# Optimization experiments

Measured on AMD Instinct MI355X. Metric: run time of the kernel, lower is better.

Reference implementation:

```python
import jax, jax.numpy as jnp
import numpy as np

B, N, M, H, NH = 8, 1024, 512, 1024, 4
DH = H // NH          # 256 main attention head size
CDH = (H // 4) // 4   # 64  cross attention qk head size
EPS = 1e-12


def _ln(x, g, b):
    mu = jnp.mean(x, axis=-1, keepdims=True)
    var = jnp.mean((x - mu) ** 2, axis=-1, keepdims=True)
    return (x - mu) / jnp.sqrt(var + EPS) * g + b


def _heads(x, nh):
    b, n, d = x.shape
    return x.reshape(b, n, nh, d // nh).transpose(0, 2, 1, 3)  # [b,nh,n,dh]


def setup_inputs() -> dict:
    key = jax.random.key(0)
    ks = iter(jax.random.split(key, 64))
    nk = lambda: next(ks)
    w = lambda *s: jax.random.normal(nk(), s, jnp.float32) * 0.02
    inp = {}
    inp["hidden_states"] = jax.random.normal(nk(), (B, N, H), jnp.float32)
    inp["attention_mask"] = jnp.ones((B, N), jnp.float32)
    inp["structure_mask"] = (jax.random.uniform(nk(), (B, 3, N, N)) < 0.2).astype(jnp.float32)
    inp["Sentence_em"] = w(1, B, N, H)
    inp["entity_id_em"] = w(1, B, N, H)
    inp["cross_struct_mask"] = (jax.random.uniform(nk(), (B, 1, N, M)) < 0.3).astype(jnp.float32)
    inp["encoder_hidden_states"] = jax.random.normal(nk(), (1, B, M, H), jnp.float32)
    inp["encoder_attention_mask"] = jnp.ones((B, M), jnp.float32)
    # ---- Struct_SelfAttention params ----
    inp["Wq"] = w(H, 3 * DH); inp["bq"] = jnp.zeros(3 * DH)
    inp["Wk"] = w(H, 3 * DH); inp["bk"] = jnp.zeros(3 * DH)
    inp["Wv"] = w(H, H);      inp["bv"] = jnp.zeros(H)
    inp["Wq1"] = w(H, DH);    inp["bq1"] = jnp.zeros(DH)
    inp["Wk1"] = w(H, DH);    inp["bk1"] = jnp.zeros(DH)
    inp["ln_g"] = jnp.ones(H); inp["ln_b"] = jnp.zeros(H)
    inp["gnn_W"] = w(H, H); inp["gnn_b"] = jnp.zeros(H)
    inp["gnn_ln_g"] = jnp.ones(H); inp["gnn_ln_b"] = jnp.zeros(H)
    # ---- Cross_Attention params ----
    inp["cWq"] = w(H, H // 4); inp["cbq"] = jnp.zeros(H // 4)
    inp["cWk"] = w(H, H // 4); inp["cbk"] = jnp.zeros(H // 4)
    inp["cWv"] = w(H, H);      inp["cbv"] = jnp.zeros(H)
    inp["cWo"] = w(H, H);      inp["cbo"] = jnp.zeros(H)
    inp["cWg"] = w(2 * H, H);  inp["cbg"] = jnp.full((H,), -1.0, jnp.float32)  # Gate bias init -1
    inp["c_ln_g"] = jnp.ones(H); inp["c_ln_b"] = jnp.zeros(H)
    # ---- Output block params ----
    inp["oW1"] = w(H, H); inp["ob1"] = jnp.zeros(H)
    inp["o_ln1_g"] = jnp.ones(H); inp["o_ln1_b"] = jnp.zeros(H)
    inp["oW2"] = w(H, 2 * H); inp["ob2"] = jnp.zeros(2 * H)
    inp["oW3"] = w(2 * H, H); inp["ob3"] = jnp.zeros(H)
    inp["o_ln3_g"] = jnp.ones(H); inp["o_ln3_b"] = jnp.zeros(H)
    inp["layer_idx"] = 0
    return inp


def reference(hidden_states, attention_mask, structure_mask, Sentence_em, entity_id_em,
              cross_struct_mask, encoder_hidden_states, encoder_attention_mask,
              Wq, bq, Wk, bk, Wv, bv, Wq1, bq1, Wk1, bk1, ln_g, ln_b,
              gnn_W, gnn_b, gnn_ln_g, gnn_ln_b,
              cWq, cbq, cWk, cbk, cWv, cbv, cWo, cbo, cWg, cbg, c_ln_g, c_ln_b,
              oW1, ob1, o_ln1_g, o_ln1_b, oW2, ob2, oW3, ob3, o_ln3_g, o_ln3_b,
              layer_idx):
    hs = hidden_states
    q = _heads(hs @ Wq + bq, 3)          # [B,3,N,DH]
    k = _heads(hs @ Wk + bk, 3)
    v = _heads(hs @ Wv + bv, 4)          # [B,4,N,DH]
    s1 = jnp.einsum('bhnd,bhmd->bhnm', q, k)          # unscaled scores, 3 heads
    am0 = (1.0 - attention_mask)[:, None, None, :] * -10000.0
    s3 = s1 + am0
    # valid off-diagonal pairs mask (broadcasts over the 3 heads)
    pair = attention_mask[:, None, :, None] * attention_mask[:, None, None, :]
    idxw = ((pair * (1.0 - jnp.eye(N, dtype=jnp.float32))) > 0.5).astype(jnp.float32)  # [B,1,N,N]
    # sigmoid focal loss (gamma=2, alpha=0.25, mean over selected elements)
    p = jax.nn.sigmoid(s3)
    t = structure_mask
    fl = 0.25 * t * (1.0 - p) ** 2 * (-jax.nn.log_sigmoid(s3)) \
       + 0.75 * (1.0 - t) * p ** 2 * (-jax.nn.log_sigmoid(-s3))
    loss = jnp.sum(fl * idxw) / (3.0 * jnp.sum(idxw))
    # structural attention path (3 heads)
    s1 = s1 / np.float32(np.sqrt(DH)) + (1.0 - structure_mask) * -10000.0
    probs1 = jax.nn.softmax(s1, axis=-1)
    # positional/structural single-head path
    h1 = _ln(hs + Sentence_em[layer_idx] + entity_id_em[layer_idx], ln_g, ln_b)
    q1 = _heads(h1 @ Wq1 + bq1, 1)
    k1 = _heads(h1 @ Wk1 + bk1, 1)
    s2 = jnp.einsum('bhnd,bhmd->bhnm', q1, k1) / np.float32(np.sqrt(DH)) + am0
    probs2 = jax.nn.softmax(s2, axis=-1)
    probs = jnp.concatenate([probs2, probs1], axis=1)  # [B,4,N,N]
    ctx = jnp.einsum('bhnm,bhmd->bhnd', probs, v).transpose(0, 2, 1, 3).reshape(B, N, H)
    gnn_out = _ln(ctx @ gnn_W + gnn_b, gnn_ln_g, gnn_ln_b)
    # ---- Cross attention ----
    enc = encoder_hidden_states[layer_idx]            # [B,M,H]
    cq = _heads(gnn_out @ cWq + cbq, 4)               # [B,4,N,CDH]
    ck = _heads(enc @ cWk + cbk, 4)                   # [B,4,M,CDH]
    cv = _heads(enc @ cWv + cbv, 4)                   # [B,4,M,DH]
    cs = jnp.einsum('bhnd,bhmd->bhnm', cq, ck) / np.float32(np.sqrt(CDH))
    cs = cs + (1.0 - cross_struct_mask) * -10000.0
    cp = jax.nn.softmax(cs, axis=-1)
    cctx = jnp.einsum('bhnm,bhmd->bhnd', cp, cv).transpose(0, 2, 1, 3).reshape(B, N, H)
    cctx = cctx @ cWo + cbo
    gate = jax.nn.sigmoid(jnp.concatenate([gnn_out, cctx], axis=-1) @ cWg + cbg)
    cross_out = _ln(gate * cctx + (1.0 - gate) * gnn_out, c_ln_g, c_ln_b)
    # ---- Output block (gated FFN) ----
    h = _ln(cross_out @ oW1 + ob1 + hidden_states, o_ln1_g, o_ln1_b)
    h3 = jax.nn.gelu(h @ oW2 + ob2, approximate=False) @ oW3 + ob3
    out = _ln(h3 + h, o_ln3_g, o_ln3_b)
    return out, loss
```

## Files before the change

### kernel.cpp

```cpp
#include <hip/hip_runtime.h>
#include <math.h>

#define DEV __device__ __forceinline__

typedef short short8 __attribute__((ext_vector_type(8)));
typedef float float4v __attribute__((ext_vector_type(4)));

DEV unsigned short f2bf(float f) {
    union { float f; unsigned u; } v; v.f = f;
    unsigned r = v.u + 0x7FFFu + ((v.u >> 16) & 1u);
    return (unsigned short)(r >> 16);
}

DEV void async16(const unsigned short* g, unsigned short* l) {
    __builtin_amdgcn_global_load_lds(
        (const __attribute__((address_space(1))) unsigned int*)g,
        (__attribute__((address_space(3))) unsigned int*)l, 16, 0, 0);
}

DEV float block_reduce(float v, int mode) {
    #pragma unroll
    for (int off = 32; off; off >>= 1) {
        float o = __shfl_xor(v, off);
        v = mode ? fmaxf(v, o) : (v + o);
    }
    __shared__ float sbuf[4];
    __syncthreads();
    if ((threadIdx.x & 63) == 0) sbuf[threadIdx.x >> 6] = v;
    __syncthreads();
    float r = sbuf[0];
    #pragma unroll
    for (int w = 1; w < 4; w++) r = mode ? fmaxf(r, sbuf[w]) : (r + sbuf[w]);
    return r;
}

template <bool BIAS, bool ACCUM, bool GELU>
__global__ __launch_bounds__(256) void gemm_bf16_kernel(
    const unsigned short* __restrict__ A, int lda,
    const unsigned short* __restrict__ Bt, int ldb,
    const float* __restrict__ bias, const float* __restrict__ bias2,
    const float* __restrict__ bias3, int ns1, int ns2,
    float* __restrict__ Cf, unsigned short* __restrict__ Cb,
    int N, int Nb, int K)
{
    __shared__ unsigned short As[128 * 32];
    __shared__ unsigned short Bs[128 * 32];
    const int tid = threadIdx.x;
    const int w = tid >> 6, lane = tid & 63;
    const int l15 = lane & 15, quad = lane >> 4;
    const int m0 = blockIdx.y * 128, n0 = blockIdx.x * 128;
    const int wm = (w >> 1) * 64, wn = (w & 1) * 64;
    const int lr = lane >> 2, lc = (lane & 3) * 8;

    float4v acc[4][4];
    #pragma unroll
    for (int i = 0; i < 4; i++)
        #pragma unroll
        for (int j = 0; j < 4; j++) acc[i][j] = (float4v){0.f, 0.f, 0.f, 0.f};

    const unsigned short* Ab = A  + (size_t)(m0 + w * 16 + lr) * lda + lc;
    const unsigned short* Bb = Bt + (size_t)(n0 + w * 16 + lr) * ldb + lc;
    unsigned short* AsW = As + (w * 16) * 32;
    unsigned short* BsW = Bs + (w * 16) * 32;

    for (int k0 = 0; k0 < K; k0 += 32) {
        __syncthreads();
        async16(Ab + k0, AsW);
        async16(Ab + (size_t)64 * lda + k0, AsW + 64 * 32);
        async16(Bb + k0, BsW);
        async16(Bb + (size_t)64 * ldb + k0, BsW + 64 * 32);
        __syncthreads();
        short8 Af[4], Bf[4];
        #pragma unroll
        for (int mt = 0; mt < 4; mt++)
            Af[mt] = *(const short8*)(As + (wm + mt * 16 + l15) * 32 + quad * 8);
        #pragma unroll
        for (int nt = 0; nt < 4; nt++)
            Bf[nt] = *(const short8*)(Bs + (wn + nt * 16 + l15) * 32 + quad * 8);
        #pragma unroll
        for (int mt = 0; mt < 4; mt++)
            #pragma unroll
            for (int nt = 0; nt < 4; nt++)
                acc[mt][nt] = __builtin_amdgcn_mfma_f32_16x16x32_bf16(
                    Af[mt], Bf[nt], acc[mt][nt], 0, 0, 0);
    }

    #pragma unroll
    for (int nt = 0; nt < 4; nt++) {
        const int n = n0 + wn + nt * 16 + l15;
        float bv = 0.f;
        if (BIAS) bv = (n < ns1) ? bias[n] : (n < ns2) ? bias2[n - ns1]
                                                       : bias3[n - ns2];
        #pragma unroll
        for (int mt = 0; mt < 4; mt++) {
            #pragma unroll
            for (int r = 0; r < 4; r++) {
                const int m = m0 + wm + mt * 16 + quad * 4 + r;
                const size_t off = (size_t)m * N + n;
                float v = acc[mt][nt][r] + bv;
                if (ACCUM) v += Cf[off];
                if (GELU) v = 0.5f * v * (1.f + erff(v * 0.70710678118654752f));
                if (Cf) Cf[off] = v;
                if (Cb) Cb[(size_t)m * Nb + n] = f2bf(v);
            }
        }
    }
}

__global__ __launch_bounds__(256) void wtrans_kernel(
    const float* __restrict__ W, unsigned short* __restrict__ Wt, int K, int N)
{
    __shared__ float t[32][33];
    const int n0 = blockIdx.x * 32, k0 = blockIdx.y * 32;
    const int c = threadIdx.x & 31, r8 = threadIdx.x >> 5;
    #pragma unroll
    for (int i = 0; i < 4; i++) {
        const int r = r8 + i * 8;
        t[r][c] = W[(size_t)(k0 + r) * N + n0 + c];
    }
    __syncthreads();
    #pragma unroll
    for (int i = 0; i < 4; i++) {
        const int r = r8 + i * 8;
        Wt[(size_t)(n0 + r) * K + k0 + c] = f2bf(t[c][r]);
    }
}

__global__ __launch_bounds__(256) void trans_kernel(
    const unsigned short* __restrict__ v, unsigned short* __restrict__ Vt,
    int R, int C, int vpitch, int voff)
{
    __shared__ unsigned short t[32][33];
    const int b = blockIdx.z, r0 = blockIdx.x * 32, c0 = blockIdx.y * 32;
    const int c = threadIdx.x & 31, r8 = threadIdx.x >> 5;
    #pragma unroll
    for (int i = 0; i < 4; i++) {
        const int r = r8 + i * 8;
        t[r][c] = v[((size_t)b * R + r0 + r) * vpitch + voff + c0 + c];
    }
    __syncthreads();
    #pragma unroll
    for (int i = 0; i < 4; i++) {
        const int r = r8 + i * 8;
        Vt[((size_t)b * C + c0 + r) * R + r0 + c] = t[c][r];
    }
}

__global__ __launch_bounds__(256) void castbf_kernel(
    const float* __restrict__ x, unsigned short* __restrict__ y)
{
    const size_t i = ((size_t)blockIdx.x * 256 + threadIdx.x) * 4;
    float4 v = *(const float4*)(x + i);
    ushort4 o;
    o.x = f2bf(v.x); o.y = f2bf(v.y); o.z = f2bf(v.z); o.w = f2bf(v.w);
    *(ushort4*)(y + i) = o;
}

__global__ __launch_bounds__(256) void packmask_kernel(
    const float* __restrict__ x, unsigned int* __restrict__ bits)
{
    const size_t idx = (size_t)blockIdx.x * 256 + threadIdx.x;
    const unsigned long long m = __ballot(x[idx] > 0.5f);
    const int lane = threadIdx.x & 63;
    if (lane == 0)  bits[idx >> 5] = (unsigned)m;
    if (lane == 32) bits[idx >> 5] = (unsigned)(m >> 32);
}

DEV void ln_finish(float4 xv, const float* __restrict__ g,
                   const float* __restrict__ bb, float* __restrict__ outf,
                   unsigned short* __restrict__ outb, size_t base_f, size_t base_b)
{
    float s  = xv.x + xv.y + xv.z + xv.w;
    float s2 = xv.x * xv.x + xv.y * xv.y + xv.z * xv.z + xv.w * xv.w;
    #pragma unroll
    for (int off = 32; off; off >>= 1) {
        s += __shfl_xor(s, off);
        s2 += __shfl_xor(s2, off);
    }
    __shared__ float sa[4], sb[4];
    if ((threadIdx.x & 63) == 0) {
        sa[threadIdx.x >> 6] = s; sb[threadIdx.x >> 6] = s2;
    }
    __syncthreads();
    s  = sa[0] + sa[1] + sa[2] + sa[3];
    s2 = sb[0] + sb[1] + sb[2] + sb[3];
    const float mu  = s * (1.f / 1024.f);
    const float var = fmaxf(s2 * (1.f / 1024.f) - mu * mu, 0.f);
    const float inv = rsqrtf(var + 1e-12f);
    const int tid = threadIdx.x;
    float4 gv = ((const float4*)g)[tid];
    float4 bv = ((const float4*)bb)[tid];
    float4 o;
    o.x = (xv.x - mu) * inv * gv.x + bv.x;
    o.y = (xv.y - mu) * inv * gv.y + bv.y;
    o.z = (xv.z - mu) * inv * gv.z + bv.z;
    o.w = (xv.w - mu) * inv * gv.w + bv.w;
    if (outf) ((float4*)(outf + base_f))[tid] = o;
    if (outb) {
        ushort4 ob;
        ob.x = f2bf(o.x); ob.y = f2bf(o.y); ob.z = f2bf(o.z); ob.w = f2bf(o.w);
        ((ushort4*)(outb + base_b))[tid] = ob;
    }
}

__global__ __launch_bounds__(256) void ln_kernel(
    const float* __restrict__ x, const float* __restrict__ r1,
    const float* __restrict__ r2, const float* __restrict__ g,
    const float* __restrict__ bb, float* __restrict__ outf,
    unsigned short* __restrict__ outb, int obp)
{
    const size_t base = (size_t)blockIdx.x * 1024;
    const size_t base_b = (size_t)blockIdx.x * obp;
    const int tid = threadIdx.x;
    float4 xv = ((const float4*)(x + base))[tid];
    if (r1) {
        float4 a = ((const float4*)(r1 + base))[tid];
        xv.x += a.x; xv.y += a.y; xv.z += a.z; xv.w += a.w;
    }
    if (r2) {
        float4 a = ((const float4*)(r2 + base))[tid];
        xv.x += a.x; xv.y += a.y; xv.z += a.z; xv.w += a.w;
    }
    ln_finish(xv, g, bb, outf, outb, base, base_b);
}

__global__ __launch_bounds__(256) void gate_ln_kernel(
    const float* __restrict__ gpre, const float* __restrict__ co,
    const float* __restrict__ gn, const float* __restrict__ g,
    const float* __restrict__ bb, float* __restrict__ outf,
    unsigned short* __restrict__ outb)
{
    const size_t base = (size_t)blockIdx.x * 1024;
    const int tid = threadIdx.x;
    float4 gp = ((const float4*)(gpre + base))[tid];
    float4 cv = ((const float4*)(co + base))[tid];
    float4 gv = ((const float4*)(gn + base))[tid];
    float4 xv; float s;
    s = 1.f / (1.f + __expf(-gp.x)); xv.x = s * cv.x + (1.f - s) * gv.x;
    s = 1.f / (1.f + __expf(-gp.y)); xv.y = s * cv.y + (1.f - s) * gv.y;
    s = 1.f / (1.f + __expf(-gp.z)); xv.z = s * cv.z + (1.f - s) * gv.z;
    s = 1.f / (1.f + __expf(-gp.w)); xv.w = s * cv.w + (1.f - s) * gv.w;
    ln_finish(xv, g, bb, outf, outb, base, base);
}

__global__ __launch_bounds__(256) void attn_mfma_kernel(
    const unsigned short* __restrict__ qkv,
    const unsigned short* __restrict__ q1k1,
    const unsigned short* __restrict__ Vt,
    const float* __restrict__ am,
    const unsigned int* __restrict__ smb,
    unsigned short* __restrict__ ctx,
    float* __restrict__ nump, float* __restrict__ denp)
{
    const int bid0 = blockIdx.x + 16 * blockIdx.y + 64 * blockIdx.z;
    const int xcd = bid0 & 7, s = bid0 >> 3;
    const int grp = xcd + 8 * (s >> 4);
    const int nb = s & 15;
    const int h = grp & 3, b = grp >> 2;
    const int tid = threadIdx.x;
    const int w = tid >> 6, lane = tid & 63;
    const int l15 = lane & 15, quad = lane >> 4;
    const int n0 = nb * 64;

    __shared__ unsigned short Ks[32 * 264];
    __shared__ unsigned short Vs[256 * 40];
    __shared__ unsigned short Ps[4][16 * 40];

    const unsigned short* qsrc; const unsigned short* ksrc; int pitch;
    if (h == 0) { qsrc = q1k1;                ksrc = q1k1 + 256;                pitch = 512; }
    else        { qsrc = qkv + (h - 1) * 256; ksrc = qkv + 768 + (h - 1) * 256; pitch = 2560; }

    short8 Qf[8];
    {
        const unsigned short* qrow =
            qsrc + (size_t)(b * 1024 + n0 + w * 16 + l15) * pitch;
        #pragma unroll
        for (int kk = 0; kk < 8; kk++)
            Qf[kk] = *(const short8*)(qrow + kk * 32 + quad * 8);
    }

    float4v O[16];
    #pragma unroll
    for (int i = 0; i < 16; i++) O[i] = (float4v){0.f, 0.f, 0.f, 0.f};
    float lsum[4] = {0.f, 0.f, 0.f, 0.f};
    float flsum = 0.f, dencnt = 0.f;
    const int nrow_base = n0 + w * 16 + quad * 4;
    const float* amrow = am + b * 1024;
    float amn[4];
    #pragma unroll
    for (int r = 0; r < 4; r++) amn[r] = amrow[nrow_base + r];
    const unsigned int* smw = (h > 0)
        ? smb + ((size_t)(b * 3 + (h - 1)) << 15) : nullptr;
    const int vrow0 = b * 1024 + h * 256;

    for (int m0 = 0; m0 < 1024; m0 += 32) {
        __syncthreads();
        for (int c = tid; c < 1024; c += 256) {
            const int row = c >> 5, kc = (c & 31) * 8;
            *(uint4*)(Ks + row * 264 + kc) =
                *(const uint4*)(ksrc + (size_t)(b * 1024 + m0 + row) * pitch + kc);
        }
        for (int c = tid; c < 1024; c += 256) {
            const int d = c >> 2, mc = (c & 3) * 8;
            *(uint4*)(Vs + d * 40 + mc) =
                *(const uint4*)(Vt + (size_t)(vrow0 + d) * 1024 + m0 + mc);
        }
        __syncthreads();

        float4v S[2];
        #pragma unroll
        for (int st = 0; st < 2; st++) {
            float4v a = (float4v){0.f, 0.f, 0.f, 0.f};
            #pragma unroll
            for (int kk = 0; kk < 8; kk++) {
                short8 Kf = *(const short8*)(Ks + (st * 16 + l15) * 264 + kk * 32 + quad * 8);
                a = __builtin_amdgcn_mfma_f32_16x16x32_bf16(Qf[kk], Kf, a, 0, 0, 0);
            }
            S[st] = a;
        }

        unsigned int wb[4];
        if (h > 0) {
            #pragma unroll
            for (int r = 0; r < 4; r++)
                wb[r] = smw[(size_t)(nrow_base + r) * 32 + (m0 >> 5)];
        }

        float e[2][4];
        #pragma unroll
        for (int st = 0; st < 2; st++) {
            const int mcol = m0 + st * 16 + l15;
            const float amm = amrow[mcol];
            const float am0 = (1.f - amm) * (-10000.f);
            #pragma unroll
            for (int r = 0; r < 4; r++) {
                const float sraw = S[st][r];
                float scv;
                if (h > 0) {
                    const float t = (float)((wb[r] >> (st * 16 + l15)) & 1u);
                    const int nrow = nrow_base + r;
                    const float s3 = sraw + am0;
                    const float idxw =
                        ((amn[r] * amm * ((mcol == nrow) ? 0.f : 1.f)) > 0.5f) ? 1.f : 0.f;
                    const float E = __expf(-fabsf(s3));
                    const float L = __logf(1.f + E);
                    const float R = 1.f / (1.f + E);
                    const float p = (s3 >= 0.f) ? R : E * R;
                    const float sp = fmaxf(s3, 0.f) + L;
                    const float omp = 1.f - p;
                    flsum += idxw * (0.25f * t * omp * omp * (sp - s3)
                                   + 0.75f * (1.f - t) * p * p * sp);
                    dencnt += idxw;
                    scv = sraw * 0.0625f + (1.f - t) * (-10000.f);
                } else {
                    scv = sraw * 0.0625f + am0;
                }
                const float ev = __expf(fminf(scv, 30.f));
                e[st][r] = ev;
                lsum[r] += ev;
            }
        }

        #pragma unroll
        for (int st = 0; st < 2; st++)
            #pragma unroll
            for (int r = 0; r < 4; r++)
                Ps[w][(quad * 4 + r) * 40 + st * 16 + l15] = f2bf(e[st][r]);
        const short8 Pf = *(const short8*)(&Ps[w][l15 * 40 + quad * 8]);
        #pragma unroll
        for (int dt = 0; dt < 16; dt++) {
            short8 Vf = *(const short8*)(Vs + (dt * 16 + l15) * 40 + quad * 8);
            O[dt] = __builtin_amdgcn_mfma_f32_16x16x32_bf16(Pf, Vf, O[dt], 0, 0, 0);
        }
    }

    float rinv[4];
    #pragma unroll
    for (int r = 0; r < 4; r++) {
        float s2 = lsum[r];
        #pragma unroll
        for (int off = 8; off; off >>= 1) s2 += __shfl_xor(s2, off);
        rinv[r] = 1.f / s2;
    }
    #pragma unroll
    for (int dt = 0; dt < 16; dt++)
        #pragma unroll
        for (int r = 0; r < 4; r++)
            ctx[(size_t)(b * 1024 + nrow_base + r) * 1024 + h * 256 + dt * 16 + l15]
                = f2bf(O[dt][r] * rinv[r]);

    if (h > 0) {
        const float fb = block_reduce(flsum, 0);
        if (tid == 0) nump[(b * 3 + (h - 1)) * 16 + nb] = fb;
        if (h == 1) {
            const float db = block_reduce(dencnt, 0);
            if (tid == 0) denp[b * 16 + nb] = db;
        }
    }
}

__global__ __launch_bounds__(256) void cross_mfma_kernel(
    const unsigned short* __restrict__ cq,
    const unsigned short* __restrict__ ckv,
    const unsigned short* __restrict__ cvt,
    const unsigned int* __restrict__ csmb,
    unsigned short* __restrict__ cctx)
{
    const int bid0 = blockIdx.x + 16 * blockIdx.y + 64 * blockIdx.z;
    const int xcd = bid0 & 7, s = bid0 >> 3;
    const int grp = xcd + 8 * (s >> 4);
    const int nb = s & 15;
    const int h = grp & 3, b = grp >> 2;
    const int tid = threadIdx.x;
    const int w = tid >> 6, lane = tid & 63;
    const int l15 = lane & 15, quad = lane >> 4;
    const int n0 = nb * 64;

    __shared__ unsigned short Ks[32 * 72];
    __shared__ unsigned short Vs[256 * 40];
    __shared__ unsigned short Ps[4][16 * 40];

    short8 Qf[2];
    {
        const unsigned short* qrow =
            cq + (size_t)(b * 1024 + n0 + w * 16 + l15) * 256 + h * 64;
        #pragma unroll
        for (int kk = 0; kk < 2; kk++)
            Qf[kk] = *(const short8*)(qrow + kk * 32 + quad * 8);
    }

    float4v O[16];
    #pragma unroll
    for (int i = 0; i < 16; i++) O[i] = (float4v){0.f, 0.f, 0.f, 0.f};
    float lsum[4] = {0.f, 0.f, 0.f, 0.f};
    const int nrow_base = n0 + w * 16 + quad * 4;
    const unsigned int* csw = csmb + (size_t)(b * 1024) * 16;
    const int vrow0 = b * 1024 + h * 256;

    for (int m0 = 0; m0 < 512; m0 += 32) {
        __syncthreads();
        {
            const int row = tid >> 3, kc = (tid & 7) * 8;
            *(uint4*)(Ks + row * 72 + kc) =
                *(const uint4*)(ckv + (size_t)(b * 512 + m0 + row) * 1280 + h * 64 + kc);
        }
        for (int c = tid; c < 1024; c += 256) {
            const int d = c >> 2, mc = (c & 3) * 8;
            *(uint4*)(Vs + d * 40 + mc) =
                *(const uint4*)(cvt + (size_t)(vrow0 + d) * 512 + m0 + mc);
        }
        __syncthreads();

        float4v S[2];
        #pragma unroll
        for (int st = 0; st < 2; st++) {
            float4v a = (float4v){0.f, 0.f, 0.f, 0.f};
            #pragma unroll
            for (int kk = 0; kk < 2; kk++) {
                short8 Kf = *(const short8*)(Ks + (st * 16 + l15) * 72 + kk * 32 + quad * 8);
                a = __builtin_amdgcn_mfma_f32_16x16x32_bf16(Qf[kk], Kf, a, 0, 0, 0);
            }
            S[st] = a;
        }

        unsigned int wb[4];
        #pragma unroll
        for (int r = 0; r < 4; r++)
            wb[r] = csw[(size_t)(nrow_base + r) * 16 + (m0 >> 5)];

        float e[2][4];
        #pragma unroll
        for (int st = 0; st < 2; st++) {
            #pragma unroll
            for (int r = 0; r < 4; r++) {
                const float msk = (float)((wb[r] >> (st * 16 + l15)) & 1u);
                const float scv = S[st][r] * 0.125f + (1.f - msk) * (-10000.f);
                const float ev = __expf(fminf(scv, 30.f));
                e[st][r] = ev;
                lsum[r] += ev;
            }
        }

        #pragma unroll
        for (int st = 0; st < 2; st++)
            #pragma unroll
            for (int r = 0; r < 4; r++)
                Ps[w][(quad * 4 + r) * 40 + st * 16 + l15] = f2bf(e[st][r]);
        const short8 Pf = *(const short8*)(&Ps[w][l15 * 40 + quad * 8]);
        #pragma unroll
        for (int dt = 0; dt < 16; dt++) {
            short8 Vf = *(const short8*)(Vs + (dt * 16 + l15) * 40 + quad * 8);
            O[dt] = __builtin_amdgcn_mfma_f32_16x16x32_bf16(Pf, Vf, O[dt], 0, 0, 0);
        }
    }

    float rinv[4];
    #pragma unroll
    for (int r = 0; r < 4; r++) {
        float s2 = lsum[r];
        #pragma unroll
        for (int off = 8; off; off >>= 1) s2 += __shfl_xor(s2, off);
        rinv[r] = 1.f / s2;
    }
    #pragma unroll
    for (int dt = 0; dt < 16; dt++)
        #pragma unroll
        for (int r = 0; r < 4; r++)
            cctx[(size_t)(b * 1024 + nrow_base + r) * 1024 + h * 256 + dt * 16 + l15]
                = f2bf(O[dt][r] * rinv[r]);
}

__global__ __launch_bounds__(256) void loss_reduce_kernel(
    const float* __restrict__ nump, const float* __restrict__ denp,
    float* __restrict__ out)
{
    __shared__ double sn[256], sd[256];
    const int tid = threadIdx.x;
    double ns = 0.0, ds = 0.0;
    for (int i = tid; i < 384; i += 256) ns += (double)nump[i];
    for (int i = tid; i < 128; i += 256) ds += (double)denp[i];
    sn[tid] = ns; sd[tid] = ds;
    __syncthreads();
    for (int off = 128; off; off >>= 1) {
        if (tid < off) { sn[tid] += sn[tid + off]; sd[tid] += sd[tid + off]; }
        __syncthreads();
    }
    if (tid == 0) out[0] = (float)(sn[0] / (3.0 * sd[0]));
}

extern "C" void kernel_launch(void* const* d_in, const int* in_sizes, int n_in,
                              void* d_out, int out_size, void* d_ws, size_t ws_size,
                              hipStream_t stream)
{
    (void)in_sizes; (void)n_in; (void)out_size; (void)ws_size;
    const float* hs   = (const float*)d_in[0];
    const float* am   = (const float*)d_in[1];
    const float* smask= (const float*)d_in[2];
    const float* sent = (const float*)d_in[3];
    const float* ent  = (const float*)d_in[4];
    const float* csm  = (const float*)d_in[5];
    const float* enc  = (const float*)d_in[6];
    const float* Wq  = (const float*)d_in[8];  const float* bq  = (const float*)d_in[9];
    const float* Wk  = (const float*)d_in[10]; const float* bk  = (const float*)d_in[11];
    const float* Wv  = (const float*)d_in[12]; const float* bv  = (const float*)d_in[13];
    const float* Wq1 = (const float*)d_in[14]; const float* bq1 = (const float*)d_in[15];
    const float* Wk1 = (const float*)d_in[16]; const float* bk1 = (const float*)d_in[17];
    const float* ln_g= (const float*)d_in[18]; const float* ln_b= (const float*)d_in[19];
    const float* gW  = (const float*)d_in[20]; const float* gb  = (const float*)d_in[21];
    const float* gng = (const float*)d_in[22]; const float* gnb = (const float*)d_in[23];
    const float* cWq = (const float*)d_in[24]; const float* cbq = (const float*)d_in[25];
    const float* cWk = (const float*)d_in[26]; const float* cbk = (const float*)d_in[27];
    const float* cWv = (const float*)d_in[28]; const float* cbv = (const float*)d_in[29];
    const float* cWo = (const float*)d_in[30]; const float* cbo = (const float*)d_in[31];
    const float* cWg = (const float*)d_in[32]; const float* cbg = (const float*)d_in[33];
    const float* clg = (const float*)d_in[34]; const float* clb = (const float*)d_in[35];
    const float* oW1 = (const float*)d_in[36]; const float* ob1 = (const float*)d_in[37];
    const float* l1g = (const float*)d_in[38]; const float* l1b = (const float*)d_in[39];
    const float* oW2 = (const float*)d_in[40]; const float* ob2 = (const float*)d_in[41];
    const float* oW3 = (const float*)d_in[42]; const float* ob3 = (const float*)d_in[43];
    const float* l3g = (const float*)d_in[44]; const float* l3b = (const float*)d_in[45];
    float* out = (float*)d_out;

    typedef unsigned short ush;
    char* wsb = (char*)d_ws;
    ush* WT   = (ush*)wsb;
    ush* wqT  = WT;             ush* wkT  = WT + 786432;   ush* wvT  = WT + 1572864;
    ush* wq1T = WT + 2621440;   ush* wk1T = WT + 2883584;  ush* gWT_ = WT + 3145728;
    ush* cWqT = WT + 4194304;   ush* cWkT = WT + 4456448;  ush* cWvT = WT + 4718592;
    ush* cWoT = WT + 5767168;   ush* cWgT = WT + 6815744;  ush* oW1T = WT + 8912896;
    ush* oW2T = WT + 9961472;   ush* oW3T = WT + 12058624;
    (void)wkT; (void)wvT; (void)wk1T; (void)cWvT;
    ush*  hs_bf   = (ush*)(wsb + 28311552);
    ush*  enc_bf  = (ush*)(wsb + 45088768);
    ush*  qkv_bf  = (ush*)(wsb + 53477376);
    ush*  Vt      = (ush*)(wsb + 95420416);
    ush*  h1_bf   = (ush*)(wsb + 112197632);
    ush*  q1k1_bf = (ush*)(wsb + 128974848);
    ush*  ctx_bf  = (ush*)(wsb + 137363456);
    float* nump   = (float*)(wsb + 154140672);
    float* denp   = (float*)(wsb + 154142208);
    float* gnn_f  = (float*)(wsb + 154144768);
    float* gnnout_f = (float*)(wsb + 187699200);
    unsigned int* smb  = (unsigned int*)(wsb + 187699200);
    unsigned int* csmb = (unsigned int*)(wsb + 28311552);
    ush*  gc_b      = (ush*)(wsb + 112197632);
    ush*  cq_b      = (ush*)(wsb + 53477376);
    ush*  ckv_b     = (ush*)(wsb + 66060288);
    ush*  cctx_b    = (ush*)(wsb + 95420416);
    ush*  cvt       = (ush*)(wsb + 238030848);
    float* cctxo_f  = (float*)(wsb + 154144768);
    float* gatepre_f= (float*)(wsb + 45088768);
    ush*  crossout_b= (ush*)(wsb + 221253632);
    float* t_f      = (float*)(wsb + 154144768);
    float* h_f      = (float*)(wsb + 187699200);
    ush*  h_b       = (ush*)(wsb + 28311552);
    ush*  h2g_b     = (ush*)(wsb + 45088768);
    float* h3_f     = (float*)(wsb + 154144768);

    const int BIG = 1 << 30;
    dim3 blk(256);
    castbf_kernel<<<8192, blk, 0, stream>>>(hs, hs_bf);
    castbf_kernel<<<4096, blk, 0, stream>>>(enc, enc_bf);
    packmask_kernel<<<98304, blk, 0, stream>>>(smask, smb);
    wtrans_kernel<<<dim3(768/32, 1024/32), blk, 0, stream>>>(Wq, wqT, 1024, 768);
    wtrans_kernel<<<dim3(768/32, 1024/32), blk, 0, stream>>>(Wk, wkT, 1024, 768);
    wtrans_kernel<<<dim3(32, 32), blk, 0, stream>>>(Wv, wvT, 1024, 1024);
    wtrans_kernel<<<dim3(8, 32), blk, 0, stream>>>(Wq1, wq1T, 1024, 256);
    wtrans_kernel<<<dim3(8, 32), blk, 0, stream>>>(Wk1, wk1T, 1024, 256);
    wtrans_kernel<<<dim3(32, 32), blk, 0, stream>>>(gW, gWT_, 1024, 1024);
    wtrans_kernel<<<dim3(8, 32), blk, 0, stream>>>(cWq, cWqT, 1024, 256);
    wtrans_kernel<<<dim3(8, 32), blk, 0, stream>>>(cWk, cWkT, 1024, 256);
    wtrans_kernel<<<dim3(32, 32), blk, 0, stream>>>(cWv, cWvT, 1024, 1024);
    wtrans_kernel<<<dim3(32, 32), blk, 0, stream>>>(cWo, cWoT, 1024, 1024);
    wtrans_kernel<<<dim3(32, 64), blk, 0, stream>>>(cWg, cWgT, 2048, 1024);
    wtrans_kernel<<<dim3(32, 32), blk, 0, stream>>>(oW1, oW1T, 1024, 1024);
    wtrans_kernel<<<dim3(64, 32), blk, 0, stream>>>(oW2, oW2T, 1024, 2048);
    wtrans_kernel<<<dim3(32, 64), blk, 0, stream>>>(oW3, oW3T, 2048, 1024);
    gemm_bf16_kernel<true,false,false><<<dim3(20, 64), blk, 0, stream>>>(
        hs_bf, 1024, wqT, 1024, bq, bk, bv, 768, 1536, nullptr, qkv_bf, 2560, 2560, 1024);
    packmask_kernel<<<16384, blk, 0, stream>>>(csm, csmb);
    ln_kernel<<<8192, blk, 0, stream>>>(hs, sent, ent, ln_g, ln_b, nullptr, h1_bf, 1024);
    gemm_bf16_kernel<true,false,false><<<dim3(4, 64), blk, 0, stream>>>(
        h1_bf, 1024, wq1T, 1024, bq1, bk1, nullptr, 256, BIG, nullptr, q1k1_bf, 512, 512, 1024);
    trans_kernel<<<dim3(32, 32, 8), blk, 0, stream>>>(qkv_bf, Vt, 1024, 1024, 2560, 1536);
    attn_mfma_kernel<<<dim3(16, 4, 8), blk, 0, stream>>>(
        qkv_bf, q1k1_bf, Vt, am, smb, ctx_bf, nump, denp);
    loss_reduce_kernel<<<1, blk, 0, stream>>>(nump, denp, out + 8388608);
    gemm_bf16_kernel<true,false,false><<<dim3(8, 64), blk, 0, stream>>>(
        ctx_bf, 1024, gWT_, 1024, gb, nullptr, nullptr, BIG, BIG, gnn_f, nullptr, 1024, 1024, 1024);
    ln_kernel<<<8192, blk, 0, stream>>>(gnn_f, nullptr, nullptr, gng, gnb,
                                        gnnout_f, gc_b, 2048);
    gemm_bf16_kernel<true,false,false><<<dim3(2, 64), blk, 0, stream>>>(
        gc_b, 2048, cWqT, 1024, cbq, nullptr, nullptr, BIG, BIG, nullptr, cq_b, 256, 256, 1024);
    gemm_bf16_kernel<true,false,false><<<dim3(10, 32), blk, 0, stream>>>(
        enc_bf, 1024, cWkT, 1024, cbk, cbv, nullptr, 256, BIG, nullptr, ckv_b, 1280, 1280, 1024);
    trans_kernel<<<dim3(16, 32, 8), blk, 0, stream>>>(ckv_b, cvt, 512, 1024, 1280, 256);
    cross_mfma_kernel<<<dim3(16, 4, 8), blk, 0, stream>>>(
        cq_b, ckv_b, cvt, csmb, cctx_b);
    gemm_bf16_kernel<true,false,false><<<dim3(8, 64), blk, 0, stream>>>(
        cctx_b, 1024, cWoT, 1024, cbo, nullptr, nullptr, BIG, BIG, cctxo_f, gc_b + 1024, 1024, 2048, 1024);
    gemm_bf16_kernel<true,false,false><<<dim3(8, 64), blk, 0, stream>>>(
        gc_b, 2048, cWgT, 2048, cbg, nullptr, nullptr, BIG, BIG, gatepre_f, nullptr, 1024, 1024, 2048);
    gate_ln_kernel<<<8192, blk, 0, stream>>>(gatepre_f, cctxo_f, gnnout_f,
                                             clg, clb, nullptr, crossout_b);
    gemm_bf16_kernel<true,false,false><<<dim3(8, 64), blk, 0, stream>>>(
        crossout_b, 1024, oW1T, 1024, ob1, nullptr, nullptr, BIG, BIG, t_f, nullptr, 1024, 1024, 1024);
    ln_kernel<<<8192, blk, 0, stream>>>(t_f, hs, nullptr, l1g, l1b, h_f, h_b, 1024);
    gemm_bf16_kernel<true,false,true><<<dim3(16, 64), blk, 0, stream>>>(
        h_b, 1024, oW2T, 1024, ob2, nullptr, nullptr, BIG, BIG, nullptr, h2g_b, 2048, 2048, 1024);
    gemm_bf16_kernel<true,false,false><<<dim3(8, 64), blk, 0, stream>>>(
        h2g_b, 2048, oW3T, 2048, ob3, nullptr, nullptr, BIG, BIG, h3_f, nullptr, 1024, 1024, 2048);
    ln_kernel<<<8192, blk, 0, stream>>>(h3_f, h_f, nullptr, l3g, l3b, out, nullptr, 1024);
}
```

Baseline: 1.207 ms.

## Double-buffer K/V LDS tiles with register prefetch in attention kernels

Both the structured self-attention and cross-attention kernels now keep two LDS buffers for the K and V tiles. The next tile is loaded from global memory into registers at the top of each iteration and written to the alternate buffer after the MFMA work. This is meant to hide global load latency behind compute and removes one of the two barriers per iteration. The cost is double the K/V LDS footprint and extra registers for the prefetched data, which could lower occupancy.

```diff
diff --git a/kernel.cpp b/kernel.cpp
--- a/kernel.cpp
+++ b/kernel.cpp
@@ -262,8 +262,8 @@
     const int l15 = lane & 15, quad = lane >> 4;
     const int n0 = nb * 64;
 
-    __shared__ unsigned short Ks[32 * 264];
-    __shared__ unsigned short Vs[256 * 40];
+    __shared__ unsigned short Ks[2][32 * 264];
+    __shared__ unsigned short Vs[2][256 * 40];
     __shared__ unsigned short Ps[4][16 * 40];
 
     const unsigned short* qsrc; const unsigned short* ksrc; int pitch;
@@ -277,6 +277,20 @@
         #pragma unroll
         for (int kk = 0; kk < 8; kk++)
             Qf[kk] = *(const short8*)(qrow + kk * 32 + quad * 8);
+    }
+
+    const unsigned short* kap[4]; int kofs[4];
+    const unsigned short* vap[4]; int vofs[4];
+    const int vrow0 = b * 1024 + h * 256;
+    #pragma unroll
+    for (int i = 0; i < 4; i++) {
+        const int c = tid + i * 256;
+        const int krow = c >> 5, kc = (c & 31) * 8;
+        kap[i] = ksrc + (size_t)(b * 1024 + krow) * pitch + kc;
+        kofs[i] = krow * 264 + kc;
+        const int d = c >> 2, mc = (c & 3) * 8;
+        vap[i] = Vt + (size_t)(vrow0 + d) * 1024 + mc;
+        vofs[i] = d * 40 + mc;
     }
 
     float4v O[16];
@@ -291,21 +305,32 @@
     for (int r = 0; r < 4; r++) amn[r] = amrow[nrow_base + r];
     const unsigned int* smw = (h > 0)
         ? smb + ((size_t)(b * 3 + (h - 1)) << 15) : nullptr;
-    const int vrow0 = b * 1024 + h * 256;
+
+    uint4 kr[4], vr[4];
+    #pragma unroll
+    for (int i = 0; i < 4; i++) {
+        kr[i] = *(const uint4*)kap[i]; kap[i] += (size_t)32 * pitch;
+        vr[i] = *(const uint4*)vap[i]; vap[i] += 32;
+    }
+    #pragma unroll
+    for (int i = 0; i < 4; i++) {
+        *(uint4*)(&Ks[0][0] + kofs[i]) = kr[i];
+        *(uint4*)(&Vs[0][0] + vofs[i]) = vr[i];
+    }
+    __syncthreads();
+    int cur = 0;
 
     for (int m0 = 0; m0 < 1024; m0 += 32) {
-        __syncthreads();
-        for (int c = tid; c < 1024; c += 256) {
-            const int row = c >> 5, kc = (c & 31) * 8;
-            *(uint4*)(Ks + row * 264 + kc) =
-                *(const uint4*)(ksrc + (size_t)(b * 1024 + m0 + row) * pitch + kc);
-        }
-        for (int c = tid; c < 1024; c += 256) {
-            const int d = c >> 2, mc = (c & 3) * 8;
-            *(uint4*)(Vs + d * 40 + mc) =
-                *(const uint4*)(Vt + (size_t)(vrow0 + d) * 1024 + m0 + mc);
-        }
-        __syncthreads();
+        const bool more = (m0 + 32 < 1024);
+        if (more) {
+            #pragma unroll
+            for (int i = 0; i < 4; i++) {
+                kr[i] = *(const uint4*)kap[i]; kap[i] += (size_t)32 * pitch;
+                vr[i] = *(const uint4*)vap[i]; vap[i] += 32;
+            }
+        }
+        const unsigned short* Ksc = &Ks[cur][0];
+        const unsigned short* Vsc = &Vs[cur][0];
 
         float4v S[2];
         #pragma unroll
@@ -313,7 +338,7 @@
             float4v a = (float4v){0.f, 0.f, 0.f, 0.f};
             #pragma unroll
             for (int kk = 0; kk < 8; kk++) {
-                short8 Kf = *(const short8*)(Ks + (st * 16 + l15) * 264 + kk * 32 + quad * 8);
+                short8 Kf = *(const short8*)(Ksc + (st * 16 + l15) * 264 + kk * 32 + quad * 8);
                 a = __builtin_amdgcn_mfma_f32_16x16x32_bf16(Qf[kk], Kf, a, 0, 0, 0);
             }
             S[st] = a;
@@ -369,8 +394,20 @@
         const short8 Pf = *(const short8*)(&Ps[w][l15 * 40 + quad * 8]);
         #pragma unroll
         for (int dt = 0; dt < 16; dt++) {
-            short8 Vf = *(const short8*)(Vs + (dt * 16 + l15) * 40 + quad * 8);
+            short8 Vf = *(const short8*)(Vsc + (dt * 16 + l15) * 40 + quad * 8);
             O[dt] = __builtin_amdgcn_mfma_f32_16x16x32_bf16(Pf, Vf, O[dt], 0, 0, 0);
+        }
+
+        if (more) {
+            unsigned short* Ksn = &Ks[cur ^ 1][0];
+            unsigned short* Vsn = &Vs[cur ^ 1][0];
+            #pragma unroll
+            for (int i = 0; i < 4; i++) {
+                *(uint4*)(Ksn + kofs[i]) = kr[i];
+                *(uint4*)(Vsn + vofs[i]) = vr[i];
+            }
+            __syncthreads();
+            cur ^= 1;
         }
     }
 
@@ -416,8 +453,8 @@
     const int l15 = lane & 15, quad = lane >> 4;
     const int n0 = nb * 64;
 
-    __shared__ unsigned short Ks[32 * 72];
-    __shared__ unsigned short Vs[256 * 40];
+    __shared__ unsigned short Ks[2][32 * 72];
+    __shared__ unsigned short Vs[2][256 * 40];
     __shared__ unsigned short Ps[4][16 * 40];
 
     short8 Qf[2];
@@ -429,27 +466,45 @@
             Qf[kk] = *(const short8*)(qrow + kk * 32 + quad * 8);
     }
 
+    const int vrow0 = b * 1024 + h * 256;
+    const int krow = tid >> 3, kc = (tid & 7) * 8;
+    const unsigned short* kap = ckv + (size_t)(b * 512 + krow) * 1280 + h * 64 + kc;
+    const int kofs = krow * 72 + kc;
+    const unsigned short* vap[4]; int vofs[4];
+    #pragma unroll
+    for (int i = 0; i < 4; i++) {
+        const int c = tid + i * 256;
+        const int d = c >> 2, mc = (c & 3) * 8;
+        vap[i] = cvt + (size_t)(vrow0 + d) * 512 + mc;
+        vofs[i] = d * 40 + mc;
+    }
+
     float4v O[16];
     #pragma unroll
     for (int i = 0; i < 16; i++) O[i] = (float4v){0.f, 0.f, 0.f, 0.f};
     float lsum[4] = {0.f, 0.f, 0.f, 0.f};
     const int nrow_base = n0 + w * 16 + quad * 4;
     const unsigned int* csw = csmb + (size_t)(b * 1024) * 16;
-    const int vrow0 = b * 1024 + h * 256;
+
+    uint4 kr, vr[4];
+    kr = *(const uint4*)kap; kap += (size_t)32 * 1280;
+    #pragma unroll
+    for (int i = 0; i < 4; i++) { vr[i] = *(const uint4*)vap[i]; vap[i] += 32; }
+    *(uint4*)(&Ks[0][0] + kofs) = kr;
+    #pragma unroll
+    for (int i = 0; i < 4; i++) *(uint4*)(&Vs[0][0] + vofs[i]) = vr[i];
+    __syncthreads();
+    int cur = 0;
 
     for (int m0 = 0; m0 < 512; m0 += 32) {
-        __syncthreads();
-        {
-            const int row = tid >> 3, kc = (tid & 7) * 8;
-            *(uint4*)(Ks + row * 72 + kc) =
-                *(const uint4*)(ckv + (size_t)(b * 512 + m0 + row) * 1280 + h * 64 + kc);
-        }
-        for (int c = tid; c < 1024; c += 256) {
-            const int d = c >> 2, mc = (c & 3) * 8;
-            *(uint4*)(Vs + d * 40 + mc) =
-                *(const uint4*)(cvt + (size_t)(vrow0 + d) * 512 + m0 + mc);
-        }
-        __syncthreads();
+        const bool more = (m0 + 32 < 512);
+        if (more) {
+            kr = *(const uint4*)kap; kap += (size_t)32 * 1280;
+            #pragma unroll
+            for (int i = 0; i < 4; i++) { vr[i] = *(const uint4*)vap[i]; vap[i] += 32; }
+        }
+        const unsigned short* Ksc = &Ks[cur][0];
+        const unsigned short* Vsc = &Vs[cur][0];
 
         float4v S[2];
         #pragma unroll
@@ -457,7 +512,7 @@
             float4v a = (float4v){0.f, 0.f, 0.f, 0.f};
             #pragma unroll
             for (int kk = 0; kk < 2; kk++) {
-                short8 Kf = *(const short8*)(Ks + (st * 16 + l15) * 72 + kk * 32 + quad * 8);
+                short8 Kf = *(const short8*)(Ksc + (st * 16 + l15) * 72 + kk * 32 + quad * 8);
                 a = __builtin_amdgcn_mfma_f32_16x16x32_bf16(Qf[kk], Kf, a, 0, 0, 0);
             }
             S[st] = a;
@@ -489,8 +544,18 @@
         const short8 Pf = *(const short8*)(&Ps[w][l15 * 40 + quad * 8]);
         #pragma unroll
         for (int dt = 0; dt < 16; dt++) {
-            short8 Vf = *(const short8*)(Vs + (dt * 16 + l15) * 40 + quad * 8);
+            short8 Vf = *(const short8*)(Vsc + (dt * 16 + l15) * 40 + quad * 8);
             O[dt] = __builtin_amdgcn_mfma_f32_16x16x32_bf16(Pf, Vf, O[dt], 0, 0, 0);
+        }
+
+        if (more) {
+            unsigned short* Ksn = &Ks[cur ^ 1][0];
+            unsigned short* Vsn = &Vs[cur ^ 1][0];
+            *(uint4*)(Ksn + kofs) = kr;
+            #pragma unroll
+            for (int i = 0; i < 4; i++) *(uint4*)(Vsn + vofs[i]) = vr[i];
+            __syncthreads();
+            cur ^= 1;
         }
     }
 
```

Result: slower. 1.277 ms (+5.8%).

## Double-buffer K/V tiles with async global-to-LDS loads in attention kernels

Applied to the files above, without the earlier changes.

Both the struct-attention and cross-attention MFMA kernels now prefetch the next K and V tiles into a second LDS buffer using global_load_lds async copies while the current tile is computed. This replaces the synchronous register-staged loads and cuts the two barriers per iteration down to one. The LDS layout changes so each wave's 16-byte async chunks land contiguously, with the K row pitch set to 528 and the V rows unpadded at 32. The unpadded V layout may introduce LDS bank conflicts, and the doubled LDS footprint may lower occupancy. Correctness relies on the barrier also waiting for the async loads to complete.

```diff
diff --git a/kernel.cpp b/kernel.cpp
--- a/kernel.cpp
+++ b/kernel.cpp
@@ -262,8 +262,8 @@
     const int l15 = lane & 15, quad = lane >> 4;
     const int n0 = nb * 64;
 
-    __shared__ unsigned short Ks[32 * 264];
-    __shared__ unsigned short Vs[256 * 40];
+    __shared__ unsigned short Ks[2][16 * 528];
+    __shared__ unsigned short Vs[2][256 * 32];
     __shared__ unsigned short Ps[4][16 * 40];
 
     const unsigned short* qsrc; const unsigned short* ksrc; int pitch;
@@ -277,6 +277,15 @@
         #pragma unroll
         for (int kk = 0; kk < 8; kk++)
             Qf[kk] = *(const short8*)(qrow + kk * 32 + quad * 8);
+    }
+
+    const int vrow0 = b * 1024 + h * 256;
+    const unsigned short* kp[4]; const unsigned short* vp[4];
+    #pragma unroll
+    for (int j = 0; j < 4; j++) {
+        const int c = w * 4 + j;
+        kp[j] = ksrc + (size_t)(b * 1024 + 2 * c + (lane >> 5)) * pitch + (lane & 31) * 8;
+        vp[j] = Vt + (size_t)(vrow0 + 16 * c + (lane >> 2)) * 1024 + (lane & 3) * 8;
     }
 
     float4v O[16];
@@ -291,29 +300,40 @@
     for (int r = 0; r < 4; r++) amn[r] = amrow[nrow_base + r];
     const unsigned int* smw = (h > 0)
         ? smb + ((size_t)(b * 3 + (h - 1)) << 15) : nullptr;
-    const int vrow0 = b * 1024 + h * 256;
+
+    #pragma unroll
+    for (int j = 0; j < 4; j++) {
+        const int c = w * 4 + j;
+        async16(kp[j], &Ks[0][c * 528]);
+        async16(vp[j], &Vs[0][c * 512]);
+        kp[j] += (size_t)32 * pitch; vp[j] += 32;
+    }
+    __syncthreads();
+    int cur = 0;
 
     for (int m0 = 0; m0 < 1024; m0 += 32) {
-        __syncthreads();
-        for (int c = tid; c < 1024; c += 256) {
-            const int row = c >> 5, kc = (c & 31) * 8;
-            *(uint4*)(Ks + row * 264 + kc) =
-                *(const uint4*)(ksrc + (size_t)(b * 1024 + m0 + row) * pitch + kc);
-        }
-        for (int c = tid; c < 1024; c += 256) {
-            const int d = c >> 2, mc = (c & 3) * 8;
-            *(uint4*)(Vs + d * 40 + mc) =
-                *(const uint4*)(Vt + (size_t)(vrow0 + d) * 1024 + m0 + mc);
-        }
-        __syncthreads();
+        const bool more = (m0 + 32 < 1024);
+        if (more) {
+            #pragma unroll
+            for (int j = 0; j < 4; j++) {
+                const int c = w * 4 + j;
+                async16(kp[j], &Ks[cur ^ 1][c * 528]);
+                async16(vp[j], &Vs[cur ^ 1][c * 512]);
+                kp[j] += (size_t)32 * pitch; vp[j] += 32;
+            }
+        }
+        const unsigned short* Ksc = &Ks[cur][0];
+        const unsigned short* Vsc = &Vs[cur][0];
 
         float4v S[2];
         #pragma unroll
         for (int st = 0; st < 2; st++) {
             float4v a = (float4v){0.f, 0.f, 0.f, 0.f};
+            const int r = st * 16 + l15;
+            const unsigned short* krow = Ksc + (r >> 1) * 528 + (r & 1) * 256;
             #pragma unroll
             for (int kk = 0; kk < 8; kk++) {
-                short8 Kf = *(const short8*)(Ks + (st * 16 + l15) * 264 + kk * 32 + quad * 8);
+                short8 Kf = *(const short8*)(krow + kk * 32 + quad * 8);
                 a = __builtin_amdgcn_mfma_f32_16x16x32_bf16(Qf[kk], Kf, a, 0, 0, 0);
             }
             S[st] = a;
@@ -369,8 +389,13 @@
         const short8 Pf = *(const short8*)(&Ps[w][l15 * 40 + quad * 8]);
         #pragma unroll
         for (int dt = 0; dt < 16; dt++) {
-            short8 Vf = *(const short8*)(Vs + (dt * 16 + l15) * 40 + quad * 8);
+            short8 Vf = *(const short8*)(Vsc + (dt * 16 + l15) * 32 + quad * 8);
             O[dt] = __builtin_amdgcn_mfma_f32_16x16x32_bf16(Pf, Vf, O[dt], 0, 0, 0);
+        }
+
+        if (more) {
+            __syncthreads();
+            cur ^= 1;
         }
     }
 
@@ -416,8 +441,8 @@
     const int l15 = lane & 15, quad = lane >> 4;
     const int n0 = nb * 64;
 
-    __shared__ unsigned short Ks[32 * 72];
-    __shared__ unsigned short Vs[256 * 40];
+    __shared__ unsigned short Ks[2][4 * 528];
+    __shared__ unsigned short Vs[2][256 * 32];
     __shared__ unsigned short Ps[4][16 * 40];
 
     short8 Qf[2];
@@ -429,35 +454,56 @@
             Qf[kk] = *(const short8*)(qrow + kk * 32 + quad * 8);
     }
 
+    const int vrow0 = b * 1024 + h * 256;
+    const unsigned short* kp =
+        ckv + (size_t)(b * 512 + 8 * w + (lane >> 3)) * 1280 + h * 64 + (lane & 7) * 8;
+    const unsigned short* vp[4];
+    #pragma unroll
+    for (int j = 0; j < 4; j++) {
+        const int c = w * 4 + j;
+        vp[j] = cvt + (size_t)(vrow0 + 16 * c + (lane >> 2)) * 512 + (lane & 3) * 8;
+    }
+
     float4v O[16];
     #pragma unroll
     for (int i = 0; i < 16; i++) O[i] = (float4v){0.f, 0.f, 0.f, 0.f};
     float lsum[4] = {0.f, 0.f, 0.f, 0.f};
     const int nrow_base = n0 + w * 16 + quad * 4;
     const unsigned int* csw = csmb + (size_t)(b * 1024) * 16;
-    const int vrow0 = b * 1024 + h * 256;
+
+    async16(kp, &Ks[0][w * 528]);
+    kp += (size_t)32 * 1280;
+    #pragma unroll
+    for (int j = 0; j < 4; j++) {
+        async16(vp[j], &Vs[0][(w * 4 + j) * 512]);
+        vp[j] += 32;
+    }
+    __syncthreads();
+    int cur = 0;
 
     for (int m0 = 0; m0 < 512; m0 += 32) {
-        __syncthreads();
-        {
-            const int row = tid >> 3, kc = (tid & 7) * 8;
-            *(uint4*)(Ks + row * 72 + kc) =
-                *(const uint4*)(ckv + (size_t)(b * 512 + m0 + row) * 1280 + h * 64 + kc);
-        }
-        for (int c = tid; c < 1024; c += 256) {
-            const int d = c >> 2, mc = (c & 3) * 8;
-            *(uint4*)(Vs + d * 40 + mc) =
-                *(const uint4*)(cvt + (size_t)(vrow0 + d) * 512 + m0 + mc);
-        }
-        __syncthreads();
+        const bool more = (m0 + 32 < 512);
+        if (more) {
+            async16(kp, &Ks[cur ^ 1][w * 528]);
+            kp += (size_t)32 * 1280;
+            #pragma unroll
+            for (int j = 0; j < 4; j++) {
+                async16(vp[j], &Vs[cur ^ 1][(w * 4 + j) * 512]);
+                vp[j] += 32;
+            }
+        }
+        const unsigned short* Ksc = &Ks[cur][0];
+        const unsigned short* Vsc = &Vs[cur][0];
 
         float4v S[2];
         #pragma unroll
         for (int st = 0; st < 2; st++) {
             float4v a = (float4v){0.f, 0.f, 0.f, 0.f};
+            const int r = st * 16 + l15;
+            const unsigned short* krow = Ksc + (r >> 3) * 528 + (r & 7) * 64;
             #pragma unroll
             for (int kk = 0; kk < 2; kk++) {
-                short8 Kf = *(const short8*)(Ks + (st * 16 + l15) * 72 + kk * 32 + quad * 8);
+                short8 Kf = *(const short8*)(krow + kk * 32 + quad * 8);
                 a = __builtin_amdgcn_mfma_f32_16x16x32_bf16(Qf[kk], Kf, a, 0, 0, 0);
             }
             S[st] = a;
@@ -489,8 +535,13 @@
         const short8 Pf = *(const short8*)(&Ps[w][l15 * 40 + quad * 8]);
         #pragma unroll
         for (int dt = 0; dt < 16; dt++) {
-            short8 Vf = *(const short8*)(Vs + (dt * 16 + l15) * 40 + quad * 8);
+            short8 Vf = *(const short8*)(Vsc + (dt * 16 + l15) * 32 + quad * 8);
             O[dt] = __builtin_amdgcn_mfma_f32_16x16x32_bf16(Pf, Vf, O[dt], 0, 0, 0);
+        }
+
+        if (more) {
+            __syncthreads();
+            cur ^= 1;
         }
     }
 
```

After: 1.157 ms. 4.2% less time.
